# Kernel optimization log

Hardware: AMD Instinct MI355X
Metric: run time of the kernel (lower is better)

The kernel has to match this reference:

```python
import jax, jax.numpy as jnp
import numpy as np

OUTLINER_RATIO = 0.01
SUB_OUTLINER_BIT = 8
NEG_INF = -1e9


def setup_inputs() -> dict:
    key = jax.random.key(0)
    T, H, D = 4096, 8, 64
    qkv = jax.random.normal(key, (T, 3, H, D), dtype=jnp.float32)
    cu_seqlens = jnp.array([0, 1024, 2048, 3072, 4096], dtype=jnp.int32)
    return {"qkv": qkv, "cu_seqlens": cu_seqlens, "max_seqlen": 1024}


def _varlen_attention(q, k, v, cu_seqlens, causal=False):
    # q,k,v: [T, H, D]; sequences delimited by cu_seqlens (attention never
    # crosses segment boundaries, matching flash_attn_varlen semantics).
    T, H, D = q.shape
    scale = D ** (-0.5)
    pos = jnp.arange(T)
    seg = jnp.searchsorted(cu_seqlens, pos, side="right") - 1  # [T] segment ids
    mask = seg[:, None] == seg[None, :]                          # [T, T]
    if causal:
        mask = mask & (pos[:, None] >= pos[None, :])
    scores = jnp.einsum("thd,shd->hts", q, k) * scale            # [H, T, T]
    scores = jnp.where(mask[None, :, :], scores, NEG_INF)
    probs = jax.nn.softmax(scores, axis=-1)
    out = jnp.einsum("hts,shd->thd", probs, v)                   # [T, H, D]
    return out


def _outlier_quant_compress(x, outliner_ratio=OUTLINER_RATIO, bit=SUB_OUTLINER_BIT):
    # Outlier detection: keep top-ratio |x| entries in full precision;
    # quantize the residual (sub-outliers) to `bit` bits per-tensor.
    a = jnp.abs(x)
    thr = jnp.quantile(a.reshape(-1), 1.0 - outliner_ratio)
    outliers = jnp.where(a > thr, x, 0.0)
    resid = x - outliers
    qmax = 2.0 ** (bit - 1) - 1.0
    scale = jnp.maximum(jnp.max(jnp.abs(resid)), 1e-8) / qmax
    q = jnp.clip(jnp.round(resid / scale), -qmax, qmax)
    x_hat = outliers + q * scale  # decompressed approximation
    return x_hat, thr, scale


def reference(qkv, cu_seqlens, max_seqlen):
    q, k, v = qkv[:, 0], qkv[:, 1], qkv[:, 2]
    out = _varlen_attention(q, k, v, cu_seqlens, causal=False)
    # Compression pipeline (stats + quantize) runs on Q,K,V,O in the original
    # forward; it does not alter the forward output.
    for t in (q, k, v, out):
        _outlier_quant_compress(t)
    return out
```

## Files before the change

### kernel.cpp

```cpp
#include <hip/hip_runtime.h>


#define HEADS 8
#define DH 64
#define TQ 64
#define TK 64
#define PSTR 72
#define NEG_BIG -1e30f
#define L2E 1.44269504088896340736f

using f32x4 = __attribute__((ext_vector_type(4))) float;
using s16x8 = __attribute__((ext_vector_type(8))) short;

__device__ inline unsigned short bf16b(float x) {
    union { float f; unsigned u; } c; c.f = x;
    unsigned r = c.u + 0x7fffu + ((c.u >> 16) & 1u);
    return (unsigned short)(r >> 16);
}

#if __has_builtin(__builtin_amdgcn_cvt_pk_bf16_f32)
__device__ inline unsigned pk2(float a, float b) {
    auto v = __builtin_amdgcn_cvt_pk_bf16_f32(a, b);
    unsigned u; __builtin_memcpy(&u, &v, 4); return u;
}
#else
__device__ inline unsigned pk2(float a, float b) {
    return (unsigned)bf16b(a) | ((unsigned)bf16b(b) << 16);
}
#endif

__global__ __launch_bounds__(256)
void prep_kernel(const float* __restrict__ qkv, unsigned short* __restrict__ Kb,
                 unsigned short* __restrict__ Vtb, int T) {
    __shared__ unsigned short Lt[64][PSTR];
    const int m = 1 + blockIdx.z, h = blockIdx.y, t0 = blockIdx.x * 64;
    const int tid = threadIdx.x, d8 = tid & 7, tr = tid >> 3;

    #pragma unroll
    for (int i = 0; i < 2; ++i) {
        int t = t0 + i * 32 + tr;
        int tc = t < T ? t : T - 1;
        const float* src = qkv + ((size_t)tc * 3 + m) * (HEADS * DH) + h * DH + d8 * 8;
        float4 a = *(const float4*)src;
        float4 b = *(const float4*)(src + 4);
        unsigned p0 = pk2(a.x, a.y), p1 = pk2(a.z, a.w);
        unsigned p2 = pk2(b.x, b.y), p3 = pk2(b.z, b.w);
        if (m == 2) {
            *(uint2*)&Lt[i * 32 + tr][d8 * 8]     = make_uint2(p0, p1);
            *(uint2*)&Lt[i * 32 + tr][d8 * 8 + 4] = make_uint2(p2, p3);
        } else if (t < T) {
            unsigned short* dst = Kb + ((size_t)h * T + t) * DH + d8 * 8;
            *(uint4*)dst = make_uint4(p0, p1, p2, p3);
        }
    }
    if (m == 2) {
        __syncthreads();
        const int d = tid >> 2, tg = tid & 3;
        #pragma unroll
        for (int p = 0; p < 2; ++p) {
            int G = tg + 4 * p;
            int td = t0 + G * 8;
            unsigned u[4];
            #pragma unroll
            for (int jj = 0; jj < 4; ++jj)
                u[jj] = (unsigned)Lt[G * 8 + 2 * jj][d] |
                        ((unsigned)Lt[G * 8 + 2 * jj + 1][d] << 16);
            if (td < T)
                *(uint4*)(Vtb + ((size_t)h * DH + d) * T + td) =
                    make_uint4(u[0], u[1], u[2], u[3]);
        }
    }
}

__global__ __launch_bounds__(256, 2)
void fa_main(const float* __restrict__ qkv, const unsigned short* __restrict__ Kb,
             const unsigned short* __restrict__ Vtb, const int* __restrict__ cu,
             int n_cu, int T, float* __restrict__ out) {
    __shared__ unsigned short Ksh0[TK * DH];
    __shared__ unsigned short Ksh1[TK * DH];
    __shared__ unsigned short Vsh0[DH * TK];
    __shared__ unsigned short Vsh1[DH * TK];
    __shared__ unsigned short Psh[TQ][PSTR];

    const int tid = threadIdx.x;
    const int h = blockIdx.y, t0 = blockIdx.x * TQ;
    const int w = tid >> 6, lane = tid & 63, n15 = lane & 15, quad = lane >> 4;

    int trow = t0 + w * 16 + n15; if (trow > T - 1) trow = T - 1;
    int lo, hi;
    { int s = 0; for (int j = 1; j < n_cu - 1; ++j) if (cu[j] <= trow) s = j;
      lo = cu[s]; hi = cu[s + 1]; }
    int kb_, ke;
    { int s = 0; for (int j = 1; j < n_cu - 1; ++j) if (cu[j] <= t0) s = j;
      kb_ = cu[s];
      int tl = t0 + TQ - 1; if (tl > T - 1) tl = T - 1;
      s = 0; for (int j = 1; j < n_cu - 1; ++j) if (cu[j] <= tl) s = j;
      ke = cu[s + 1]; }

    s16x8 qfrag[2];
    {
        int tc = t0 + w * 16 + n15; if (tc > T - 1) tc = T - 1;
        const float* qp = qkv + (size_t)tc * 3 * (HEADS * DH) + h * DH;
        #pragma unroll
        for (int f = 0; f < 2; ++f) {
            const float* p = qp + f * 32 + quad * 8;
            float4 a = *(const float4*)p;
            float4 b = *(const float4*)(p + 4);
            union { unsigned u[4]; s16x8 v; } cv;
            cv.u[0] = pk2(a.x * 0.125f, a.y * 0.125f);
            cv.u[1] = pk2(a.z * 0.125f, a.w * 0.125f);
            cv.u[2] = pk2(b.x * 0.125f, b.y * 0.125f);
            cv.u[3] = pk2(b.z * 0.125f, b.w * 0.125f);
            qfrag[f] = cv.v;
        }
    }

    const unsigned short* kb_h = Kb + (size_t)h * T * DH;
    const unsigned short* vt_h = Vtb + (size_t)h * DH * T;
    int krow_rel[2], vkey_off[2];
    const unsigned short* kbase[2];
    const unsigned short* vbase[2];
    #pragma unroll
    for (int i = 0; i < 2; ++i) {
        int gg = i * 64 + lane;
        int rr = gg >> 3;
        int gc = gg & 7;
        int row = w * 16 + rr;
        int gcol = gc ^ (row & 7);
        krow_rel[i] = row;
        kbase[i] = kb_h + gcol * 8;
        vbase[i] = vt_h + (size_t)row * T;
        vkey_off[i] = gcol * 8;
    }
    int off16[2];
    #pragma unroll
    for (int kh = 0; kh < 2; ++kh)
        off16[kh] = n15 * 128 + (((kh * 4 + quad) ^ (n15 & 7)) * 16);

    f32x4 oacc[4];
    #pragma unroll
    for (int i = 0; i < 4; ++i) oacc[i] = (f32x4){0.f, 0.f, 0.f, 0.f};
    float m_ = NEG_BIG, l_ = 0.f;

    auto STAGE = [&](unsigned short* Kd, unsigned short* Vd, int c0s) {
        #pragma unroll
        for (int i = 0; i < 2; ++i) {
            int rk = c0s + krow_rel[i]; if (rk > T - 1) rk = T - 1;
            __builtin_amdgcn_global_load_lds(
                (const __attribute__((address_space(1))) void*)(kbase[i] + ((size_t)rk << 6)),
                (__attribute__((address_space(3))) void*)&Kd[(w * 128 + i * 64) * 8],
                16, 0, 0);
            int kv = c0s + vkey_off[i]; if (kv > T - 8) kv = T - 8;
            __builtin_amdgcn_global_load_lds(
                (const __attribute__((address_space(1))) void*)(vbase[i] + kv),
                (__attribute__((address_space(3))) void*)&Vd[(w * 128 + i * 64) * 8],
                16, 0, 0);
        }
    };

    auto COMPUTE = [&](const unsigned short* Ks, const unsigned short* Vs, int c0) {
        const char* Kc = (const char*)Ks;
        f32x4 sacc[4];
        __builtin_amdgcn_s_setprio(1);
        #pragma unroll
        for (int nt = 0; nt < 4; ++nt) {
            s16x8 k0 = *(const s16x8*)(Kc + nt * 2048 + off16[0]);
            s16x8 k1 = *(const s16x8*)(Kc + nt * 2048 + off16[1]);
            f32x4 z = (f32x4){0.f, 0.f, 0.f, 0.f};
            z = __builtin_amdgcn_mfma_f32_16x16x32_bf16(k0, qfrag[0], z, 0, 0, 0);
            z = __builtin_amdgcn_mfma_f32_16x16x32_bf16(k1, qfrag[1], z, 0, 0, 0);
            sacc[nt] = z;
        }
        __builtin_amdgcn_s_setprio(0);

        if (!(c0 >= lo && c0 + TK <= hi)) {
            #pragma unroll
            for (int nt = 0; nt < 4; ++nt)
                #pragma unroll
                for (int reg = 0; reg < 4; ++reg) {
                    int key = c0 + nt * 16 + quad * 4 + reg;
                    bool valid = (key >= lo) && (key < hi);
                    sacc[nt][reg] = valid ? sacc[nt][reg] : NEG_BIG;
                }
        }

        float rm = NEG_BIG;
        #pragma unroll
        for (int nt = 0; nt < 4; ++nt)
            #pragma unroll
            for (int reg = 0; reg < 4; ++reg) rm = fmaxf(rm, sacc[nt][reg]);
        rm = fmaxf(rm, __shfl_xor(rm, 16));
        rm = fmaxf(rm, __shfl_xor(rm, 32));

        if (__any(rm > m_)) {
            float mn = fmaxf(m_, rm);
            float alpha = exp2f((m_ - mn) * L2E);
            l_ *= alpha;
            m_ = mn;
            #pragma unroll
            for (int reg = 0; reg < 4; ++reg) {
                float ar = __shfl(alpha, quad * 4 + reg);
                oacc[0][reg] *= ar; oacc[1][reg] *= ar;
                oacc[2][reg] *= ar; oacc[3][reg] *= ar;
            }
        }
        float mnl = m_ * L2E;
        float rs = 0.f;
        #pragma unroll
        for (int nt = 0; nt < 4; ++nt) {
            float p0 = exp2f(fmaf(sacc[nt][0], L2E, -mnl));
            float p1 = exp2f(fmaf(sacc[nt][1], L2E, -mnl));
            float p2 = exp2f(fmaf(sacc[nt][2], L2E, -mnl));
            float p3 = exp2f(fmaf(sacc[nt][3], L2E, -mnl));
            rs += (p0 + p1) + (p2 + p3);
            *(uint2*)&Psh[w * 16 + n15][nt * 16 + quad * 4] =
                make_uint2(pk2(p0, p1), pk2(p2, p3));
        }
        rs += __shfl_xor(rs, 16);
        rs += __shfl_xor(rs, 32);
        l_ += rs;

        s16x8 afr[2];
        afr[0] = *(const s16x8*)&Psh[w * 16 + n15][quad * 8];
        afr[1] = *(const s16x8*)&Psh[w * 16 + n15][32 + quad * 8];
        const char* Vc = (const char*)Vs;
        __builtin_amdgcn_s_setprio(1);
        #pragma unroll
        for (int nt = 0; nt < 4; ++nt) {
            s16x8 v0 = *(const s16x8*)(Vc + nt * 2048 + off16[0]);
            s16x8 v1 = *(const s16x8*)(Vc + nt * 2048 + off16[1]);
            oacc[nt] = __builtin_amdgcn_mfma_f32_16x16x32_bf16(afr[0], v0, oacc[nt], 0, 0, 0);
            oacc[nt] = __builtin_amdgcn_mfma_f32_16x16x32_bf16(afr[1], v1, oacc[nt], 0, 0, 0);
        }
        __builtin_amdgcn_s_setprio(0);
    };

    const int nIter = (ke - kb_) / TK;
    int c0 = kb_;
    int rem = nIter;

    STAGE(Ksh0, Vsh0, c0);
    __syncthreads();

    for (;;) {
        if (rem > 1) STAGE(Ksh1, Vsh1, c0 + TK);
        COMPUTE(Ksh0, Vsh0, c0);
        __syncthreads();
        if (--rem == 0) break;
        c0 += TK;

        if (rem > 1) STAGE(Ksh0, Vsh0, c0 + TK);
        COMPUTE(Ksh1, Vsh1, c0);
        __syncthreads();
        if (--rem == 0) break;
        c0 += TK;
    }

    #pragma unroll
    for (int reg = 0; reg < 4; ++reg) {
        float lr = __shfl(l_, quad * 4 + reg);
        float inv = 1.f / fmaxf(lr, 1e-30f);
        int t = t0 + w * 16 + quad * 4 + reg;
        if (t < T) {
            #pragma unroll
            for (int nt = 0; nt < 4; ++nt)
                out[((size_t)t * HEADS + h) * DH + nt * 16 + n15] = oacc[nt][reg] * inv;
        }
    }
}

extern "C" void kernel_launch(void* const* d_in, const int* in_sizes, int n_in,
                              void* d_out, int out_size, void* d_ws, size_t ws_size,
                              hipStream_t stream) {
    const float* qkv = (const float*)d_in[0];
    const int* cu    = (const int*)d_in[1];
    const int n_cu   = in_sizes[1];
    const int T      = in_sizes[0] / (3 * HEADS * DH);
    float* out       = (float*)d_out;

    size_t elems = (size_t)T * HEADS * DH;
    unsigned short* Kb  = (unsigned short*)d_ws;
    unsigned short* Vtb = Kb + elems;

    int tiles = (T + TQ - 1) / TQ;
    dim3 pgrid(tiles, HEADS, 2);
    prep_kernel<<<pgrid, 256, 0, stream>>>(qkv, Kb, Vtb, T);

    dim3 grid(tiles, HEADS);
    fa_main<<<grid, 256, 0, stream>>>(qkv, Kb, Vtb, cu, n_cu, T, out);
}
```

Baseline: 102.8 us.

## Deepen K/V prefetch with explicit vmcnt waits and lazy softmax rescale

Restructures the K/V double-buffer loop so two tiles are in flight. Each iteration waits with a partial s_waitcnt vmcnt and raw s_barrier instead of __syncthreads, then issues the next-next tile's loads after compute. It also skips the online-softmax rescale unless the row max grows by more than a threshold, cutting exp and shuffle work. The vmcnt(4) count assumes a specific number of outstanding loads per STAGE, so a wrong count could cause races. The lazy rescale relies on unnormalized values staying in fp32/bf16 range.

```diff
diff --git a/kernel.cpp b/kernel.cpp
--- a/kernel.cpp
+++ b/kernel.cpp
@@ -8,6 +8,7 @@
 #define PSTR 72
 #define NEG_BIG -1e30f
 #define L2E 1.44269504088896340736f
+#define RESCALE_THR 8.0f
 
 using f32x4 = __attribute__((ext_vector_type(4))) float;
 using s16x8 = __attribute__((ext_vector_type(8))) short;
@@ -192,7 +193,7 @@
         rm = fmaxf(rm, __shfl_xor(rm, 16));
         rm = fmaxf(rm, __shfl_xor(rm, 32));
 
-        if (__any(rm > m_)) {
+        if (__any(rm > m_ + RESCALE_THR)) {
             float mn = fmaxf(m_, rm);
             float alpha = exp2f((m_ - mn) * L2E);
             l_ *= alpha;
@@ -235,24 +236,32 @@
         __builtin_amdgcn_s_setprio(0);
     };
 
+    asm volatile("s_waitcnt vmcnt(0)" ::: "memory");
+    __builtin_amdgcn_sched_barrier(0);
+
     const int nIter = (ke - kb_) / TK;
     int c0 = kb_;
-    int rem = nIter;
-
     STAGE(Ksh0, Vsh0, c0);
-    __syncthreads();
-
-    for (;;) {
-        if (rem > 1) STAGE(Ksh1, Vsh1, c0 + TK);
-        COMPUTE(Ksh0, Vsh0, c0);
-        __syncthreads();
-        if (--rem == 0) break;
-        c0 += TK;
-
-        if (rem > 1) STAGE(Ksh0, Vsh0, c0 + TK);
-        COMPUTE(Ksh1, Vsh1, c0);
-        __syncthreads();
-        if (--rem == 0) break;
+    if (nIter > 1) STAGE(Ksh1, Vsh1, c0 + TK);
+
+    for (int it = 0; it < nIter; ++it) {
+        if (it + 2 < nIter) {
+            asm volatile("s_waitcnt vmcnt(4)" ::: "memory");
+        } else {
+            asm volatile("s_waitcnt vmcnt(0)" ::: "memory");
+        }
+        __builtin_amdgcn_sched_barrier(0);
+        __builtin_amdgcn_s_barrier();
+        asm volatile("" ::: "memory");
+        if (it & 1) COMPUTE(Ksh1, Vsh1, c0);
+        else        COMPUTE(Ksh0, Vsh0, c0);
+        asm volatile("" ::: "memory");
+        __builtin_amdgcn_s_barrier();
+        asm volatile("" ::: "memory");
+        if (it + 2 < nIter) {
+            if (it & 1) STAGE(Ksh1, Vsh1, c0 + 2 * TK);
+            else        STAGE(Ksh0, Vsh0, c0 + 2 * TK);
+        }
         c0 += TK;
     }
 
```

Result: no change. 104.2 us (+1.4%).
